# Performance work log

Hardware: AMD Instinct MI355X
Metric: run time of the kernel (lower is better)

Reference implementation:

```python
import jax, jax.numpy as jnp
import numpy as np

N, E, H, C, HID = 50000, 800000, 4, 24, 96
NUM_ZONES, BATCH = 6, 64
NEG_SLOPE = 0.2


def _ln(x, scale, bias, eps=1e-5):
    m = jnp.mean(x, -1, keepdims=True)
    v = jnp.var(x, -1, keepdims=True)
    return (x - m) * jax.lax.rsqrt(v + eps) * scale + bias


def _gat_layer(x, src, dst, edge_attr, W, a_src, a_dst, We, a_edge, bias):
    # add self-loops (PyG default, fill_value='mean' -> per-dst mean of edge_attr)
    deg = jax.ops.segment_sum(jnp.ones((E,), x.dtype), dst, num_segments=N)
    loop_attr = jax.ops.segment_sum(edge_attr, dst, num_segments=N) / jnp.clip(deg, 1.0)[:, None]
    loops = jnp.arange(N, dtype=src.dtype)
    s = jnp.concatenate([src, loops])
    d = jnp.concatenate([dst, loops])
    ea = jnp.concatenate([edge_attr, loop_attr], axis=0)  # [E+N, edge_dim]

    h = (x @ W).reshape(N, H, C)                      # shared lin_src/lin_dst
    e = (ea @ We).reshape(-1, H, C)                   # edge feature projection
    a_s = jnp.einsum('nhc,hc->nh', h, a_src)
    a_d = jnp.einsum('nhc,hc->nh', h, a_dst)
    alpha = a_s[s] + a_d[d] + jnp.einsum('ehc,hc->eh', e, a_edge)  # [E+N, H]
    alpha = jnp.where(alpha > 0, alpha, NEG_SLOPE * alpha)

    # segment softmax over incoming edges of each dst node
    mx = jax.ops.segment_max(alpha, d, num_segments=N)
    ex = jnp.exp(alpha - mx[d])
    den = jax.ops.segment_sum(ex, d, num_segments=N)
    attn = ex / (den[d] + 1e-16)                      # [E+N, H]

    msg = attn[:, :, None] * h[s]                     # [E+N, H, C]
    out = jax.ops.segment_sum(msg, d, num_segments=N).reshape(N, H * C)
    return out + bias


def setup_inputs() -> dict:
    key = jax.random.key(0)
    ks = jax.random.split(key, 40)
    p = {}
    p['x'] = jax.random.normal(ks[0], (N, 12), jnp.float32)
    p['edge_index'] = jax.random.randint(ks[1], (2, E), 0, N)
    p['edge_attr'] = jax.random.normal(ks[2], (E, 4), jnp.float32)
    p['zone_idx'] = jax.random.randint(ks[3], (BATCH * NUM_ZONES,), 0, N)
    g = lambda k, s: jax.random.normal(k, s, jnp.float32) * 0.1
    p['in_w1'] = g(ks[4], (12, HID)); p['in_b1'] = jnp.zeros((HID,))
    p['in_w2'] = g(ks[5], (HID, HID)); p['in_b2'] = jnp.zeros((HID,))
    p['conv_w'] = g(ks[6], (4, HID, HID))
    p['conv_att_src'] = g(ks[7], (4, H, C))
    p['conv_att_dst'] = g(ks[8], (4, H, C))
    p['conv_lin_edge'] = g(ks[9], (4, 4, HID))
    p['conv_att_edge'] = g(ks[10], (4, H, C))
    p['conv_bias'] = jnp.zeros((4, HID))
    p['norm_scale'] = jnp.ones((4, HID)); p['norm_bias'] = jnp.zeros((4, HID))
    for i, (name, o) in enumerate([('cong', 2), ('delay', 1), ('jit', 1)]):
        p[f'{name}_w1'] = g(ks[11 + 6 * i], (HID, HID)); p[f'{name}_b1'] = jnp.zeros((HID,))
        p[f'{name}_w2'] = g(ks[12 + 6 * i], (HID, HID // 2)); p[f'{name}_b2'] = jnp.zeros((HID // 2,))
        p[f'{name}_w3'] = g(ks[13 + 6 * i], (HID // 2, o)); p[f'{name}_b3'] = jnp.zeros((o,))
    return p


def _head(z, w1, b1, w2, b2, w3, b3):
    z = jax.nn.relu(z @ w1 + b1)
    z = jax.nn.relu(z @ w2 + b2)
    return z @ w3 + b3


def reference(x, edge_index, edge_attr, zone_idx,
              in_w1, in_b1, in_w2, in_b2,
              conv_w, conv_att_src, conv_att_dst, conv_lin_edge, conv_att_edge, conv_bias,
              norm_scale, norm_bias,
              cong_w1, cong_b1, cong_w2, cong_b2, cong_w3, cong_b3,
              delay_w1, delay_b1, delay_w2, delay_b2, delay_w3, delay_b3,
              jit_w1, jit_b1, jit_w2, jit_b2, jit_w3, jit_b3):
    src, dst = edge_index[0], edge_index[1]
    h = jax.nn.relu(x @ in_w1 + in_b1) @ in_w2 + in_b2
    for i in range(4):
        res = h
        h = _gat_layer(h, src, dst, edge_attr, conv_w[i], conv_att_src[i],
                       conv_att_dst[i], conv_lin_edge[i], conv_att_edge[i], conv_bias[i])
        h = jax.nn.elu(h)
        h = _ln(h + res, norm_scale[i], norm_bias[i])
        # dropout: eval mode -> identity
    z = h[zone_idx]                                   # [BATCH*NUM_ZONES, HID]
    preds = jnp.concatenate([
        _head(z, cong_w1, cong_b1, cong_w2, cong_b2, cong_w3, cong_b3),
        _head(z, delay_w1, delay_b1, delay_w2, delay_b2, delay_w3, delay_b3),
        _head(z, jit_w1, jit_b1, jit_w2, jit_b2, jit_w3, jit_b3)], axis=-1)
    return preds.reshape(BATCH, NUM_ZONES, 4)
```

## Files before the change

### kernel.cpp

```cpp
#include <hip/hip_runtime.h>
#include <hip/hip_fp16.h>

#define NN 50000
#define EE 800000
#define HIDD 96
#define NZ 384
#define NSCAT (EE/256)
#define NGEMB ((NN+63)/64)

typedef __attribute__((ext_vector_type(8))) _Float16 half8;
typedef __attribute__((ext_vector_type(4))) float floatx4;

struct __align__(16) Rec{ int src; __half2 e01; __half2 e23; int pad; };

__global__ void k_deg(const int* __restrict__ dst, int* __restrict__ deg){
  int e=blockIdx.x*blockDim.x+threadIdx.x;
  if(e>=EE) return;
  atomicAdd(&deg[dst[e]],1);
}

__global__ void k_scan1(const int* __restrict__ deg, int* __restrict__ off, int* __restrict__ part){
  __shared__ int sd[256];
  int t=threadIdx.x, b=blockIdx.x;
  int base=b*1024+t*4;
  int v0=(base+0<NN)?deg[base+0]:0;
  int v1=(base+1<NN)?deg[base+1]:0;
  int v2=(base+2<NN)?deg[base+2]:0;
  int v3=(base+3<NN)?deg[base+3]:0;
  int s=v0+v1+v2+v3;
  sd[t]=s; __syncthreads();
  for(int o=1;o<256;o<<=1){
    int x=(t>=o)?sd[t-o]:0;
    __syncthreads();
    sd[t]+=x;
    __syncthreads();
  }
  int ep=sd[t]-s;
  if(base+0<NN) off[base+0]=ep;
  if(base+1<NN) off[base+1]=ep+v0;
  if(base+2<NN) off[base+2]=ep+v0+v1;
  if(base+3<NN) off[base+3]=ep+v0+v1+v2;
  if(t==255) part[b]=sd[255];
}

__global__ void k_scan2(int* part, int* off, int nb){
  if(threadIdx.x==0&&blockIdx.x==0){
    int run=0;
    for(int i=0;i<nb;i++){ int x=part[i]; part[i]=run; run+=x; }
    off[NN]=run;
  }
}

__global__ void k_scan3(const int* __restrict__ part, int* __restrict__ off, int* __restrict__ cur){
  int i=blockIdx.x*blockDim.x+threadIdx.x;
  if(i<NN){ int v=off[i]+part[i>>10]; off[i]=v; cur[i]=v; }
}

__global__ void k_prepw(const float* __restrict__ conv_w, const float* __restrict__ a_src,
                        const float* __restrict__ a_dst, const float* __restrict__ lin_e,
                        const float* __restrict__ a_e,
                        float* __restrict__ Watt, float* __restrict__ Mm){
  int t=blockIdx.x*blockDim.x+threadIdx.x;
  const int WT=4*96*8;
  if(t<WT){
    int l=t/(96*8); int rem=t-l*(96*8); int k=rem>>3; int j=rem&7;
    int hh=j&3;
    const float* W=conv_w+(size_t)l*96*96+(size_t)k*96;
    const float* a=((j>=4)?a_dst:a_src)+l*96+hh*24;
    float v=0.f;
    #pragma unroll
    for(int c=0;c<24;c++) v+=W[hh*24+c]*a[c];
    Watt[t]=v;
  } else if(t<WT+64){
    int q=t-WT; int l=q>>4; int i=(q>>2)&3; int hh=q&3;
    const float* We=lin_e+(size_t)l*4*96+(size_t)i*96;
    const float* a=a_e+l*96+hh*24;
    float v=0.f;
    #pragma unroll
    for(int c=0;c<24;c++) v+=We[hh*24+c]*a[c];
    Mm[q]=v;
  }
}

__global__ __launch_bounds__(256) void k_gemm96(const float* __restrict__ x,
                                                const float* __restrict__ w1,
                                                const float* __restrict__ b1,
                                                const float* __restrict__ W,
                                                const float* __restrict__ bias,
                                                float* __restrict__ C){
  __shared__ float As[64][100];
  __shared__ float Ws[96][96];
  __shared__ float b1s[96];
  int t=threadIdx.x;
  int r0=blockIdx.x*64;
  for(int i=t;i<12*96/4;i+=256) ((float4*)&Ws[0][0])[i]=((const float4*)w1)[i];
  if(t<96) b1s[t]=b1[t];
  __syncthreads();
  {
    int r=t>>2, cq=t&3;
    int g=r0+r;
    float xv[12];
    if(g<NN){
      float4 v0=*(const float4*)(x+(size_t)g*12);
      float4 v1=*(const float4*)(x+(size_t)g*12+4);
      float4 v2=*(const float4*)(x+(size_t)g*12+8);
      xv[0]=v0.x;xv[1]=v0.y;xv[2]=v0.z;xv[3]=v0.w;
      xv[4]=v1.x;xv[5]=v1.y;xv[6]=v1.z;xv[7]=v1.w;
      xv[8]=v2.x;xv[9]=v2.y;xv[10]=v2.z;xv[11]=v2.w;
    }else{
      #pragma unroll
      for(int k=0;k<12;k++) xv[k]=0.f;
    }
    const float* w1f=&Ws[0][0];
    #pragma unroll
    for(int j=0;j<24;j++){
      int c=cq+4*j;
      float a=b1s[c];
      #pragma unroll
      for(int k=0;k<12;k++) a+=xv[k]*w1f[k*96+c];
      As[r][c]=fmaxf(a,0.f);
    }
  }
  __syncthreads();
  for(int i=t;i<96*96/4;i+=256) ((float4*)&Ws[0][0])[i]=((const float4*)W)[i];
  __syncthreads();
  int cg=t&15, rg=t>>4;
  int c0=cg*6, r=rg*4;
  float acc[4][6];
  #pragma unroll
  for(int i=0;i<4;i++)
    #pragma unroll
    for(int j=0;j<6;j++) acc[i][j]=0.f;
  for(int k4=0;k4<96;k4+=4){
    float4 a0=*(float4*)&As[r  ][k4];
    float4 a1=*(float4*)&As[r+1][k4];
    float4 a2=*(float4*)&As[r+2][k4];
    float4 a3=*(float4*)&As[r+3][k4];
    #pragma unroll
    for(int kk=0;kk<4;kk++){
      float2 w01=*(float2*)&Ws[k4+kk][c0];
      float2 w23=*(float2*)&Ws[k4+kk][c0+2];
      float2 w45=*(float2*)&Ws[k4+kk][c0+4];
      float wv[6]={w01.x,w01.y,w23.x,w23.y,w45.x,w45.y};
      float av0=((float*)&a0)[kk],av1=((float*)&a1)[kk],av2=((float*)&a2)[kk],av3=((float*)&a3)[kk];
      #pragma unroll
      for(int j=0;j<6;j++){
        acc[0][j]+=av0*wv[j];
        acc[1][j]+=av1*wv[j];
        acc[2][j]+=av2*wv[j];
        acc[3][j]+=av3*wv[j];
      }
    }
  }
  #pragma unroll
  for(int i=0;i<4;i++){
    int g=r0+r+i;
    if(g<NN){
      #pragma unroll
      for(int j=0;j<6;j++) C[(size_t)g*96+c0+j]=acc[i][j]+bias[c0+j];
    }
  }
}

__device__ __forceinline__ void gemmM_body(int bid, const float* __restrict__ A,
    const float* __restrict__ W, const float* __restrict__ Watt8,
    __half* __restrict__ hp16, float* __restrict__ att, half8 (*Bl)[7][64]){
  int t=threadIdx.x;
  for(int i=t;i<3*7*64;i+=256){
    int kk=i/448; int rem=i-kk*448; int nb=rem>>6; int l=rem&63;
    int kbase=kk*32+((l>>4)<<3);
    int n=nb*16+(l&15);
    half8 v;
    #pragma unroll
    for(int j=0;j<8;j++){
      int k=kbase+j;
      float x=(n<96)?W[k*96+n]:((n<104)?Watt8[k*8+(n-96)]:0.f);
      v[j]=(_Float16)x;
    }
    Bl[kk][nb][l]=v;
  }
  __syncthreads();
  int wid=t>>6, l=t&63;
  int row0=bid*64+wid*16;
  int arow=row0+(l&15);
  bool rv=arow<NN;
  const float* Ar=A+(size_t)(rv?arow:0)*96;
  half8 a[3];
  #pragma unroll
  for(int kk=0;kk<3;kk++){
    int kb=kk*32+((l>>4)<<3);
    floatx4 lo=*(const floatx4*)(Ar+kb);
    floatx4 hi=*(const floatx4*)(Ar+kb+4);
    half8 v;
    #pragma unroll
    for(int j=0;j<4;j++){ v[j]=(_Float16)(rv?lo[j]:0.f); v[j+4]=(_Float16)(rv?hi[j]:0.f); }
    a[kk]=v;
  }
  int col16=l&15;
  int rbase=row0+((l>>4)<<2);
  #pragma unroll
  for(int nb=0;nb<7;nb++){
    floatx4 acc={0.f,0.f,0.f,0.f};
    #pragma unroll
    for(int kk=0;kk<3;kk++)
      acc=__builtin_amdgcn_mfma_f32_16x16x32_f16(a[kk],Bl[kk][nb][l],acc,0,0,0);
    int col=nb*16+col16;
    if(col<96){
      #pragma unroll
      for(int r=0;r<4;r++){
        int g=rbase+r;
        if(g<NN) hp16[(size_t)g*96+col]=__float2half(acc[r]);
      }
    } else if(col<104){
      #pragma unroll
      for(int r=0;r<4;r++){
        int g=rbase+r;
        if(g<NN) att[(size_t)g*8+(col-96)]=acc[r];
      }
    }
  }
}

__global__ __launch_bounds__(256) void k_gemmM(const float* __restrict__ A,
    const float* __restrict__ W, const float* __restrict__ Watt8,
    __half* __restrict__ hp16, float* __restrict__ att){
  __shared__ half8 Bl[3][7][64];
  gemmM_body(blockIdx.x,A,W,Watt8,hp16,att,Bl);
}

__global__ __launch_bounds__(256) void k_scat_gemmM(
    const int* __restrict__ src, const int* __restrict__ dst,
    const float* __restrict__ eattr, int* __restrict__ cur, Rec* __restrict__ rec,
    const float* __restrict__ A, const float* __restrict__ W,
    const float* __restrict__ Watt8, __half* __restrict__ hp16, float* __restrict__ att){
  __shared__ half8 Bl[3][7][64];
  int b=blockIdx.x;
  if(b<NSCAT){
    int e=b*256+threadIdx.x;
    if(e>=EE) return;
    int d=dst[e];
    int p=atomicAdd(&cur[d],1);
    float4 ea=*(const float4*)(eattr+(size_t)e*4);
    Rec r; r.src=src[e];
    r.e01=__floats2half2_rn(ea.x,ea.y);
    r.e23=__floats2half2_rn(ea.z,ea.w);
    r.pad=0;
    rec[p]=r;
    return;
  }
  gemmM_body(b-NSCAT,A,W,Watt8,hp16,att,Bl);
}

__global__ __launch_bounds__(256) void k_agg(const __half* __restrict__ hp16,
    const float* __restrict__ att, float* __restrict__ h,
    const int* __restrict__ off, const Rec* __restrict__ rec,
    const float* __restrict__ Mm, const float* __restrict__ bias,
    const float* __restrict__ nsc, const float* __restrict__ nbi){
  __shared__ float w4[16][17][4];
  __shared__ int   roA[16][17];
  int tid=threadIdx.x;
  int sg=tid>>4, sl=tid&15;
  int n=blockIdx.x*16+sg;
  if(n>=NN) return;
  float M[16];
  #pragma unroll
  for(int i=0;i<16;i++) M[i]=Mm[i];
  const float4 ad=*(const float4*)(att+(size_t)n*8+4);
  int b0=off[n], deg=off[n+1]-b0;
  float invdeg=1.f/(float)(deg>0?deg:1);
  int hL=sl>>2;
  int sloff=sl*12;
  float ds0=0.f,ds1=0.f,ds2=0.f,ds3=0.f;
  float sx=0.f,sy=0.f,sz=0.f,sw=0.f;
  float acc[6]={0.f,0.f,0.f,0.f,0.f,0.f};
  const char* hb=(const char*)hp16;

  for(int cs=0;cs<deg;cs+=16){
    int idx=cs+sl;
    bool valid=idx<deg;
    float w0=0.f,w1=0.f,w2=0.f,w3=0.f; int ro=0;
    if(valid){
      int ei=b0+idx;
      Rec rr=rec[ei];
      int s=rr.src;
      float2 e01=__half22float2(rr.e01);
      float2 e23=__half22float2(rr.e23);
      ro=s*192;
      sx+=e01.x; sy+=e01.y; sz+=e23.x; sw+=e23.y;
      const float4 as=*(const float4*)(att+(size_t)s*8);
      float a0=as.x+ad.x+e01.x*M[0]+e01.y*M[4]+e23.x*M[8] +e23.y*M[12];
      float a1=as.y+ad.y+e01.x*M[1]+e01.y*M[5]+e23.x*M[9] +e23.y*M[13];
      float a2=as.z+ad.z+e01.x*M[2]+e01.y*M[6]+e23.x*M[10]+e23.y*M[14];
      float a3=as.w+ad.w+e01.x*M[3]+e01.y*M[7]+e23.x*M[11]+e23.y*M[15];
      a0=a0>0.f?a0:0.2f*a0; a1=a1>0.f?a1:0.2f*a1;
      a2=a2>0.f?a2:0.2f*a2; a3=a3>0.f?a3:0.2f*a3;
      w0=__expf(a0); w1=__expf(a1); w2=__expf(a2); w3=__expf(a3);
      ds0+=w0; ds1+=w1; ds2+=w2; ds3+=w3;
    }
    *(float4*)&w4[sg][sl][0]=float4{w0,w1,w2,w3};
    roA[sg][sl]=ro;
    int nc=deg-cs; if(nc>16) nc=16;
    for(int jj=0;jj<nc;jj+=4){
      int m=nc-jj;
      float ev0,ev1,ev2,ev3; uint3 u0,u1,u2,u3;
      ev0=w4[sg][jj][hL];
      u0=*(const uint3*)(hb+(size_t)(unsigned)roA[sg][jj]+sloff);
      if(m>1){ ev1=w4[sg][jj+1][hL]; u1=*(const uint3*)(hb+(size_t)(unsigned)roA[sg][jj+1]+sloff); }
      if(m>2){ ev2=w4[sg][jj+2][hL]; u2=*(const uint3*)(hb+(size_t)(unsigned)roA[sg][jj+2]+sloff); }
      if(m>3){ ev3=w4[sg][jj+3][hL]; u3=*(const uint3*)(hb+(size_t)(unsigned)roA[sg][jj+3]+sloff); }
      {
        float2 f0=__half22float2(*(__half2*)&u0.x);
        float2 f1=__half22float2(*(__half2*)&u0.y);
        float2 f2=__half22float2(*(__half2*)&u0.z);
        acc[0]+=ev0*f0.x; acc[1]+=ev0*f0.y;
        acc[2]+=ev0*f1.x; acc[3]+=ev0*f1.y;
        acc[4]+=ev0*f2.x; acc[5]+=ev0*f2.y;
      }
      if(m>1){
        float2 f0=__half22float2(*(__half2*)&u1.x);
        float2 f1=__half22float2(*(__half2*)&u1.y);
        float2 f2=__half22float2(*(__half2*)&u1.z);
        acc[0]+=ev1*f0.x; acc[1]+=ev1*f0.y;
        acc[2]+=ev1*f1.x; acc[3]+=ev1*f1.y;
        acc[4]+=ev1*f2.x; acc[5]+=ev1*f2.y;
      }
      if(m>2){
        float2 f0=__half22float2(*(__half2*)&u2.x);
        float2 f1=__half22float2(*(__half2*)&u2.y);
        float2 f2=__half22float2(*(__half2*)&u2.z);
        acc[0]+=ev2*f0.x; acc[1]+=ev2*f0.y;
        acc[2]+=ev2*f1.x; acc[3]+=ev2*f1.y;
        acc[4]+=ev2*f2.x; acc[5]+=ev2*f2.y;
      }
      if(m>3){
        float2 f0=__half22float2(*(__half2*)&u3.x);
        float2 f1=__half22float2(*(__half2*)&u3.y);
        float2 f2=__half22float2(*(__half2*)&u3.z);
        acc[0]+=ev3*f0.x; acc[1]+=ev3*f0.y;
        acc[2]+=ev3*f1.x; acc[3]+=ev3*f1.y;
        acc[4]+=ev3*f2.x; acc[5]+=ev3*f2.y;
      }
    }
  }
  #pragma unroll
  for(int m=1;m<16;m<<=1){
    ds0+=__shfl_xor(ds0,m); ds1+=__shfl_xor(ds1,m);
    ds2+=__shfl_xor(ds2,m); ds3+=__shfl_xor(ds3,m);
    sx +=__shfl_xor(sx ,m); sy +=__shfl_xor(sy ,m);
    sz +=__shfl_xor(sz ,m); sw +=__shfl_xor(sw ,m);
  }
  float lx=sx*invdeg, ly=sy*invdeg, lz=sz*invdeg, lw=sw*invdeg;
  const float4 aself=*(const float4*)(att+(size_t)n*8);
  float b0a=aself.x+ad.x+lx*M[0]+ly*M[4]+lz*M[8] +lw*M[12];
  float b1a=aself.y+ad.y+lx*M[1]+ly*M[5]+lz*M[9] +lw*M[13];
  float b2a=aself.z+ad.z+lx*M[2]+ly*M[6]+lz*M[10]+lw*M[14];
  float b3a=aself.w+ad.w+lx*M[3]+ly*M[7]+lz*M[11]+lw*M[15];
  b0a=b0a>0.f?b0a:0.2f*b0a; b1a=b1a>0.f?b1a:0.2f*b1a;
  b2a=b2a>0.f?b2a:0.2f*b2a; b3a=b3a>0.f?b3a:0.2f*b3a;
  float e0=__expf(b0a),e1=__expf(b1a),e2=__expf(b2a),e3=__expf(b3a);
  ds0+=e0; ds1+=e1; ds2+=e2; ds3+=e3;
  float eL=(hL==0)?e0:((hL==1)?e1:((hL==2)?e2:e3));
  {
    const char* rp=hb+(size_t)n*192+sloff;
    uint3 u=*(const uint3*)rp;
    float2 f0=__half22float2(*(__half2*)&u.x);
    float2 f1=__half22float2(*(__half2*)&u.y);
    float2 f2=__half22float2(*(__half2*)&u.z);
    acc[0]+=eL*f0.x; acc[1]+=eL*f0.y;
    acc[2]+=eL*f1.x; acc[3]+=eL*f1.y;
    acc[4]+=eL*f2.x; acc[5]+=eL*f2.y;
  }
  float dL=(hL==0)?ds0:((hL==1)?ds1:((hL==2)?ds2:ds3));
  float rinv=1.f/(dL+1e-16f);
  const float* hrow=h+(size_t)n*HIDD+(size_t)sl*6;
  float2 r01=*(const float2*)(hrow);
  float2 r23=*(const float2*)(hrow+2);
  float2 r45=*(const float2*)(hrow+4);
  float rr[6]={r01.x,r01.y,r23.x,r23.y,r45.x,r45.y};
  const float* bp=bias+sl*6;
  float t[6];
  #pragma unroll
  for(int c=0;c<6;c++){
    float v=acc[c]*rinv+bp[c];
    v=v>0.f?v:expm1f(v);
    t[c]=v+rr[c];
  }
  float s1l=t[0]+t[1]+t[2]+t[3]+t[4]+t[5];
  float s2l=t[0]*t[0]+t[1]*t[1]+t[2]*t[2]+t[3]*t[3]+t[4]*t[4]+t[5]*t[5];
  #pragma unroll
  for(int m=1;m<16;m<<=1){ s1l+=__shfl_xor(s1l,m); s2l+=__shfl_xor(s2l,m); }
  float mean=s1l*(1.f/96.f);
  float var=s2l*(1.f/96.f)-mean*mean;
  float rs=rsqrtf(var+1e-5f);
  float* op=h+(size_t)n*HIDD+(size_t)sl*6;
  const float* sc=nsc+sl*6;
  const float* bi=nbi+sl*6;
  float o[6];
  #pragma unroll
  for(int c=0;c<6;c++) o[c]=(t[c]-mean)*rs*sc[c]+bi[c];
  *(float2*)(op)  =float2{o[0],o[1]};
  *(float2*)(op+2)=float2{o[2],o[3]};
  *(float2*)(op+4)=float2{o[4],o[5]};
}

__global__ __launch_bounds__(256) void k_hd1(const float* __restrict__ h, const int* __restrict__ zone,
    const float* __restrict__ cw1,const float* __restrict__ cb1,
    const float* __restrict__ dw1,const float* __restrict__ db1,
    const float* __restrict__ jw1,const float* __restrict__ jb1,
    float* __restrict__ t1){
  int idx=blockIdx.x*256+threadIdx.x;
  if(idx>=3*NZ*96) return;
  int hd=idx/(NZ*96); int rem=idx-hd*(NZ*96); int row=rem/96; int j=rem-row*96;
  const float* w1=(hd==0)?cw1:((hd==1)?dw1:jw1);
  const float* b1=(hd==0)?cb1:((hd==1)?db1:jb1);
  int n=zone[row];
  const float* hr=h+(size_t)n*96;
  float acc=b1[j];
  #pragma unroll
  for(int k4=0;k4<24;k4++){
    float4 hv=*(const float4*)(hr+k4*4);
    acc+=hv.x*w1[(k4*4+0)*96+j];
    acc+=hv.y*w1[(k4*4+1)*96+j];
    acc+=hv.z*w1[(k4*4+2)*96+j];
    acc+=hv.w*w1[(k4*4+3)*96+j];
  }
  t1[idx]=fmaxf(acc,0.f);
}

__global__ __launch_bounds__(256) void k_hd2(const float* __restrict__ t1,
    const float* __restrict__ cw2,const float* __restrict__ cb2,
    const float* __restrict__ dw2,const float* __restrict__ db2,
    const float* __restrict__ jw2,const float* __restrict__ jb2,
    float* __restrict__ t2){
  int idx=blockIdx.x*256+threadIdx.x;
  if(idx>=3*NZ*48) return;
  int hd=idx/(NZ*48); int rem=idx-hd*(NZ*48); int row=rem/48; int c=rem-row*48;
  const float* w2=(hd==0)?cw2:((hd==1)?dw2:jw2);
  const float* b2=(hd==0)?cb2:((hd==1)?db2:jb2);
  const float* t1r=t1+(size_t)hd*NZ*96+(size_t)row*96;
  float acc=b2[c];
  #pragma unroll
  for(int k4=0;k4<24;k4++){
    float4 tv=*(const float4*)(t1r+k4*4);
    acc+=tv.x*w2[(k4*4+0)*48+c];
    acc+=tv.y*w2[(k4*4+1)*48+c];
    acc+=tv.z*w2[(k4*4+2)*48+c];
    acc+=tv.w*w2[(k4*4+3)*48+c];
  }
  t2[idx]=fmaxf(acc,0.f);
}

__global__ __launch_bounds__(256) void k_hd3(const float* __restrict__ t2,
    const float* __restrict__ cw3,const float* __restrict__ cb3,
    const float* __restrict__ dw3,const float* __restrict__ db3,
    const float* __restrict__ jw3,const float* __restrict__ jb3,
    float* __restrict__ out){
  int idx=blockIdx.x*256+threadIdx.x;
  if(idx>=NZ*4) return;
  int row=idx>>2, o=idx&3;
  int hd=(o<2)?0:((o==2)?1:2);
  int c=(o<2)?o:0;
  int osz=(hd==0)?2:1;
  const float* w3=(hd==0)?cw3:((hd==1)?dw3:jw3);
  const float* b3=(hd==0)?cb3:((hd==1)?db3:jb3);
  const float* t2r=t2+(size_t)hd*NZ*48+(size_t)row*48;
  float acc=b3[c];
  #pragma unroll
  for(int k=0;k<48;k++) acc+=t2r[k]*w3[k*osz+c];
  out[idx]=acc;
}

extern "C" void kernel_launch(void* const* d_in, const int* in_sizes, int n_in,
                              void* d_out, int out_size, void* d_ws, size_t ws_size,
                              hipStream_t stream){
  const float* x       =(const float*)d_in[0];
  const int*   eidx    =(const int*)  d_in[1];
  const float* eattr   =(const float*)d_in[2];
  const int*   zone    =(const int*)  d_in[3];
  const float* in_w1   =(const float*)d_in[4];
  const float* in_b1   =(const float*)d_in[5];
  const float* in_w2   =(const float*)d_in[6];
  const float* in_b2   =(const float*)d_in[7];
  const float* conv_w  =(const float*)d_in[8];
  const float* att_src =(const float*)d_in[9];
  const float* att_dst =(const float*)d_in[10];
  const float* lin_edge=(const float*)d_in[11];
  const float* att_edge=(const float*)d_in[12];
  const float* conv_bias=(const float*)d_in[13];
  const float* nsc     =(const float*)d_in[14];
  const float* nbi     =(const float*)d_in[15];
  float* out=(float*)d_out;

  char* p=(char*)d_ws;
  auto carve=[&](size_t bytes)->char*{ char* r=p; p+=(bytes+255)&~(size_t)255; return r; };
  float*  h    =(float*)carve((size_t)NN*96*4);
  char*   uni  =carve((size_t)NN*96*4);
  __half* hp16 =(__half*)uni;
  float*  att  =(float*)(uni+(size_t)NN*96*2);
  Rec*    rec  =(Rec*)  carve((size_t)EE*16);
  int*    deg  =(int*)  carve((size_t)NN*4);
  int*    off  =(int*)  carve((size_t)(NN+1)*4);
  int*    cur  =(int*)  carve((size_t)NN*4);
  float*  Watt =(float*)carve((size_t)4*96*8*4);
  float*  Mm   =(float*)carve(64*4);
  int*    part =(int*)  carve(64*4);
  float*  t1b  =(float*)carve((size_t)3*NZ*96*4);
  float*  t2b  =(float*)carve((size_t)3*NZ*48*4);

  const int* srcp=eidx;
  const int* dstp=eidx+EE;

  hipMemsetAsync(deg,0,(size_t)NN*4,stream);
  k_deg<<<EE/256,256,0,stream>>>(dstp,deg);
  k_scan1<<<49,256,0,stream>>>(deg,off,part);
  k_scan2<<<1,64,0,stream>>>(part,off,49);
  k_scan3<<<(NN+255)/256,256,0,stream>>>(part,off,cur);
  k_prepw<<<(4*96*8+64+255)/256,256,0,stream>>>(conv_w,att_src,att_dst,lin_edge,att_edge,Watt,Mm);

  k_gemm96<<<NGEMB,256,0,stream>>>(x,in_w1,in_b1,in_w2,in_b2,h);

  k_scat_gemmM<<<NSCAT+NGEMB,256,0,stream>>>(srcp,dstp,eattr,cur,rec,
                                             h,conv_w,Watt,hp16,att);
  k_agg<<<(NN+15)/16,256,0,stream>>>(hp16,att,h,off,rec,Mm,
                                     conv_bias,nsc,nbi);

  for(int l=1;l<4;l++){
    k_gemmM<<<NGEMB,256,0,stream>>>(h,conv_w+(size_t)l*96*96,Watt+(size_t)l*96*8,hp16,att);
    k_agg<<<(NN+15)/16,256,0,stream>>>(hp16,att,h,off,rec,Mm+l*16,
                                       conv_bias+l*96,nsc+l*96,nbi+l*96);
  }

  k_hd1<<<(3*NZ*96+255)/256,256,0,stream>>>(h,zone,
    (const float*)d_in[16],(const float*)d_in[17],
    (const float*)d_in[22],(const float*)d_in[23],
    (const float*)d_in[28],(const float*)d_in[29], t1b);
  k_hd2<<<(3*NZ*48+255)/256,256,0,stream>>>(t1b,
    (const float*)d_in[18],(const float*)d_in[19],
    (const float*)d_in[24],(const float*)d_in[25],
    (const float*)d_in[30],(const float*)d_in[31], t2b);
  k_hd3<<<(NZ*4+255)/256,256,0,stream>>>(t2b,
    (const float*)d_in[20],(const float*)d_in[21],
    (const float*)d_in[26],(const float*)d_in[27],
    (const float*)d_in[32],(const float*)d_in[33], out);
}
```

Baseline: 365.0 us.

## Two-pass bucketed CSR scatter to localize edge record writes

The single-pass edge scatter into CSR order is replaced by two passes. The first scatters records into coarse 32-node buckets, stashing the destination in the pad field. The second re-scatters from bucket order into exact per-node slots, so its atomics and writes land in nearby memory. This also un-fuses the scatter from the first layer's GEMM, dropping the overlap, and adds a temporary 12.8MB buffer plus an extra full pass over the edges.

New measurement: 479.0 us. 31.2% more time.

```diff
diff --git a/kernel.cpp b/kernel.cpp
--- a/kernel.cpp
+++ b/kernel.cpp
@@ -5,8 +5,7 @@
 #define EE 800000
 #define HIDD 96
 #define NZ 384
-#define NSCAT (EE/256)
-#define NGEMB ((NN+63)/64)
+#define NBK ((NN+31)/32)
 
 typedef __attribute__((ext_vector_type(8))) _Float16 half8;
 typedef __attribute__((ext_vector_type(4))) float floatx4;
@@ -51,9 +50,39 @@
   }
 }
 
-__global__ void k_scan3(const int* __restrict__ part, int* __restrict__ off, int* __restrict__ cur){
+__global__ void k_scan3(const int* __restrict__ part, int* __restrict__ off,
+                        int* __restrict__ cur, int* __restrict__ bcur){
   int i=blockIdx.x*blockDim.x+threadIdx.x;
-  if(i<NN){ int v=off[i]+part[i>>10]; off[i]=v; cur[i]=v; }
+  if(i<NN){
+    int v=off[i]+part[i>>10];
+    off[i]=v; cur[i]=v;
+    if((i&31)==0) bcur[i>>5]=v;
+  }
+}
+
+__global__ void k_scat1(const int* __restrict__ src, const int* __restrict__ dst,
+                        const float* __restrict__ eattr, int* __restrict__ bcur,
+                        Rec* __restrict__ tmp){
+  int e=blockIdx.x*blockDim.x+threadIdx.x;
+  if(e>=EE) return;
+  int d=dst[e];
+  int p=atomicAdd(&bcur[d>>5],1);
+  float4 ea=*(const float4*)(eattr+(size_t)e*4);
+  Rec r; r.src=src[e];
+  r.e01=__floats2half2_rn(ea.x,ea.y);
+  r.e23=__floats2half2_rn(ea.z,ea.w);
+  r.pad=d;
+  tmp[p]=r;
+}
+
+__global__ void k_scat2(const Rec* __restrict__ tmp, int* __restrict__ cur,
+                        Rec* __restrict__ rec){
+  int i=blockIdx.x*blockDim.x+threadIdx.x;
+  if(i>=EE) return;
+  Rec r=tmp[i];
+  int d=r.pad;
+  int p=atomicAdd(&cur[d],1);
+  rec[p]=r;
 }
 
 __global__ void k_prepw(const float* __restrict__ conv_w, const float* __restrict__ a_src,
@@ -162,9 +191,10 @@
   }
 }
 
-__device__ __forceinline__ void gemmM_body(int bid, const float* __restrict__ A,
+__global__ __launch_bounds__(256) void k_gemmM(const float* __restrict__ A,
     const float* __restrict__ W, const float* __restrict__ Watt8,
-    __half* __restrict__ hp16, float* __restrict__ att, half8 (*Bl)[7][64]){
+    __half* __restrict__ hp16, float* __restrict__ att){
+  __shared__ half8 Bl[3][7][64];
   int t=threadIdx.x;
   for(int i=t;i<3*7*64;i+=256){
     int kk=i/448; int rem=i-kk*448; int nb=rem>>6; int l=rem&63;
@@ -181,7 +211,7 @@
   }
   __syncthreads();
   int wid=t>>6, l=t&63;
-  int row0=bid*64+wid*16;
+  int row0=blockIdx.x*64+wid*16;
   int arow=row0+(l&15);
   bool rv=arow<NN;
   const float* Ar=A+(size_t)(rv?arow:0)*96;
@@ -219,36 +249,6 @@
       }
     }
   }
-}
-
-__global__ __launch_bounds__(256) void k_gemmM(const float* __restrict__ A,
-    const float* __restrict__ W, const float* __restrict__ Watt8,
-    __half* __restrict__ hp16, float* __restrict__ att){
-  __shared__ half8 Bl[3][7][64];
-  gemmM_body(blockIdx.x,A,W,Watt8,hp16,att,Bl);
-}
-
-__global__ __launch_bounds__(256) void k_scat_gemmM(
-    const int* __restrict__ src, const int* __restrict__ dst,
-    const float* __restrict__ eattr, int* __restrict__ cur, Rec* __restrict__ rec,
-    const float* __restrict__ A, const float* __restrict__ W,
-    const float* __restrict__ Watt8, __half* __restrict__ hp16, float* __restrict__ att){
-  __shared__ half8 Bl[3][7][64];
-  int b=blockIdx.x;
-  if(b<NSCAT){
-    int e=b*256+threadIdx.x;
-    if(e>=EE) return;
-    int d=dst[e];
-    int p=atomicAdd(&cur[d],1);
-    float4 ea=*(const float4*)(eattr+(size_t)e*4);
-    Rec r; r.src=src[e];
-    r.e01=__floats2half2_rn(ea.x,ea.y);
-    r.e23=__floats2half2_rn(ea.z,ea.w);
-    r.pad=0;
-    rec[p]=r;
-    return;
-  }
-  gemmM_body(b-NSCAT,A,W,Watt8,hp16,att,Bl);
 }
 
 __global__ __launch_bounds__(256) void k_agg(const __half* __restrict__ hp16,
@@ -498,9 +498,11 @@
   __half* hp16 =(__half*)uni;
   float*  att  =(float*)(uni+(size_t)NN*96*2);
   Rec*    rec  =(Rec*)  carve((size_t)EE*16);
+  Rec*    tmp  =(Rec*)  carve((size_t)EE*16);
   int*    deg  =(int*)  carve((size_t)NN*4);
   int*    off  =(int*)  carve((size_t)(NN+1)*4);
   int*    cur  =(int*)  carve((size_t)NN*4);
+  int*    bcur =(int*)  carve((size_t)NBK*4);
   float*  Watt =(float*)carve((size_t)4*96*8*4);
   float*  Mm   =(float*)carve(64*4);
   int*    part =(int*)  carve(64*4);
@@ -514,18 +516,15 @@
   k_deg<<<EE/256,256,0,stream>>>(dstp,deg);
   k_scan1<<<49,256,0,stream>>>(deg,off,part);
   k_scan2<<<1,64,0,stream>>>(part,off,49);
-  k_scan3<<<(NN+255)/256,256,0,stream>>>(part,off,cur);
+  k_scan3<<<(NN+255)/256,256,0,stream>>>(part,off,cur,bcur);
+  k_scat1<<<EE/256,256,0,stream>>>(srcp,dstp,eattr,bcur,tmp);
+  k_scat2<<<EE/256,256,0,stream>>>(tmp,cur,rec);
   k_prepw<<<(4*96*8+64+255)/256,256,0,stream>>>(conv_w,att_src,att_dst,lin_edge,att_edge,Watt,Mm);
 
-  k_gemm96<<<NGEMB,256,0,stream>>>(x,in_w1,in_b1,in_w2,in_b2,h);
-
-  k_scat_gemmM<<<NSCAT+NGEMB,256,0,stream>>>(srcp,dstp,eattr,cur,rec,
-                                             h,conv_w,Watt,hp16,att);
-  k_agg<<<(NN+15)/16,256,0,stream>>>(hp16,att,h,off,rec,Mm,
-                                     conv_bias,nsc,nbi);
-
-  for(int l=1;l<4;l++){
-    k_gemmM<<<NGEMB,256,0,stream>>>(h,conv_w+(size_t)l*96*96,Watt+(size_t)l*96*8,hp16,att);
+  k_gemm96<<<(NN+63)/64,256,0,stream>>>(x,in_w1,in_b1,in_w2,in_b2,h);
+
+  for(int l=0;l<4;l++){
+    k_gemmM<<<(NN+63)/64,256,0,stream>>>(h,conv_w+(size_t)l*96*96,Watt+(size_t)l*96*8,hp16,att);
     k_agg<<<(NN+15)/16,256,0,stream>>>(hp16,att,h,off,rec,Mm+l*16,
                                        conv_bias+l*96,nsc+l*96,nbi+l*96);
   }
```
